# Kernel optimization log

Hardware: AMD Instinct MI355X
Metric: run time of the kernel (lower is better)

## Reference

```python
import jax, jax.numpy as jnp
import numpy as np

B, N, M, D = 4, 256, 256, 524
EPS = 1e-8


def setup_inputs() -> dict:
    key = jax.random.key(0)
    ks = jax.random.split(key, 16)

    def lin(k, fin, fout):
        kw, kb = jax.random.split(k)
        w = jax.random.normal(kw, (fin, fout), jnp.float32) * (1.0 / np.sqrt(fin))
        b = jax.random.normal(kb, (fout,), jnp.float32) * 0.01
        return w, b

    cw1, cb1 = lin(ks[3], D, 256)
    cw2, cb2 = lin(ks[4], 256, 128)
    cw3, cb3 = lin(ks[5], 128, 1)
    ow1, ob1 = lin(ks[6], D, 128)
    ow2, ob2 = lin(ks[7], 128, 1)
    return {
        "L_bat": jax.random.normal(ks[0], (B, N, M, D), jnp.float32),
        "src_centroids": jax.random.normal(ks[1], (B, N, 3), jnp.float32),
        "tgt_centroids": jax.random.normal(ks[2], (B, M, 3), jnp.float32),
        "cw1": cw1, "cb1": cb1, "cw2": cw2, "cb2": cb2, "cw3": cw3, "cb3": cb3,
        "ow1": ow1, "ob1": ob1, "ow2": ow2, "ob2": ob2,
    }


def _rot_mat_to_quat(R):
    # Shepperd's method, fully batched, scalar-last [x, y, z, w].
    tr = R[:, 0, 0] + R[:, 1, 1] + R[:, 2, 2]
    s0 = jnp.sqrt(jnp.maximum(tr + 1.0, 1e-10)) * 2
    q0 = jnp.stack([(R[:, 2, 1] - R[:, 1, 2]) / s0, (R[:, 0, 2] - R[:, 2, 0]) / s0,
                    (R[:, 1, 0] - R[:, 0, 1]) / s0, 0.25 * s0], axis=-1)
    s1 = jnp.sqrt(jnp.maximum(1.0 + R[:, 0, 0] - R[:, 1, 1] - R[:, 2, 2], 1e-10)) * 2
    q1 = jnp.stack([0.25 * s1, (R[:, 0, 1] + R[:, 1, 0]) / s1,
                    (R[:, 0, 2] + R[:, 2, 0]) / s1, (R[:, 2, 1] - R[:, 1, 2]) / s1], axis=-1)
    s2 = jnp.sqrt(jnp.maximum(1.0 + R[:, 1, 1] - R[:, 0, 0] - R[:, 2, 2], 1e-10)) * 2
    q2 = jnp.stack([(R[:, 0, 1] + R[:, 1, 0]) / s2, 0.25 * s2,
                    (R[:, 1, 2] + R[:, 2, 1]) / s2, (R[:, 0, 2] - R[:, 2, 0]) / s2], axis=-1)
    s3 = jnp.sqrt(jnp.maximum(1.0 + R[:, 2, 2] - R[:, 0, 0] - R[:, 1, 1], 1e-10)) * 2
    q3 = jnp.stack([(R[:, 0, 2] + R[:, 2, 0]) / s3, (R[:, 1, 2] + R[:, 2, 1]) / s3,
                    0.25 * s3, (R[:, 1, 0] - R[:, 0, 1]) / s3], axis=-1)
    c1 = (tr > 0)[:, None]
    c2 = ((R[:, 0, 0] > R[:, 1, 1]) & (R[:, 0, 0] > R[:, 2, 2]))[:, None]
    c3 = (R[:, 1, 1] > R[:, 2, 2])[:, None]
    q = jnp.where(c1, q0, jnp.where(c2, q1, jnp.where(c3, q2, q3)))
    return q / jnp.maximum(jnp.linalg.norm(q, axis=-1, keepdims=True), 1e-12)


def _forward(L_bat, src_centroids, tgt_centroids,
             cw1, cb1, cw2, cb2, cw3, cb3, ow1, ob1, ow2, ob2):
    # corr MLP: [B,N,M,D] -> [B,N,M]
    h = jax.nn.relu(L_bat @ cw1 + cb1)
    h = jax.nn.relu(h @ cw2 + cb2)
    corr_scores = (h @ cw3 + cb3)[..., 0]
    corr_weights = jax.nn.softmax(corr_scores, axis=2)              # softmax over M
    matched = jnp.einsum('bnmd,bnm->bnd', L_bat, corr_weights)      # [B,N,D]
    overlap = jax.nn.sigmoid(jax.nn.relu(matched @ ow1 + ob1) @ ow2 + ob2)  # [B,N,1]
    tgt_matched = jnp.einsum('bnm,bmc->bnc', corr_weights, tgt_centroids)   # [B,N,3]
    w = overlap[..., 0]
    w_norm = w / jnp.maximum(w.sum(axis=1, keepdims=True), EPS)
    src_bar = jnp.einsum('bn,bnc->bc', w_norm, src_centroids)
    tgt_bar = jnp.einsum('bn,bnc->bc', w_norm, tgt_matched)
    src_c = src_centroids - src_bar[:, None, :]
    tgt_c = tgt_matched - tgt_bar[:, None, :]
    H = jnp.einsum('bnc,bn,bnd->bcd', src_c, w_norm, tgt_c)          # [B,3,3]
    U, S, Vh = jnp.linalg.svd(H)
    R_raw = jnp.einsum('bki,bjk->bij', Vh, U)                        # Vh^T @ U^T
    det_sign = jnp.sign(jnp.linalg.det(R_raw))
    corr_fix = jnp.stack([jnp.ones_like(det_sign), jnp.ones_like(det_sign), det_sign], axis=-1)
    Vh_fix = Vh * corr_fix[:, :, None]
    R = jnp.einsum('bki,bjk->bij', Vh_fix, U)
    translation = tgt_bar - jnp.einsum('bij,bj->bi', R, src_bar)
    quaternion = _rot_mat_to_quat(R)
    return quaternion, translation, R, corr_weights, overlap


def reference(L_bat, src_centroids, tgt_centroids,
              cw1, cb1, cw2, cb2, cw3, cb3, ow1, ob1, ow2, ob2):
    return _forward(L_bat, src_centroids, tgt_centroids,
                    cw1, cb1, cw2, cb2, cw3, cb3, ow1, ob1, ow2, ob2)
```

## Files before the change

kernel.cpp:

```cpp
#include <hip/hip_runtime.h>
#include <hip/hip_bf16.h>


#define D_ 524
#define CW_OFF 64
#define OV_OFF 262208

typedef __attribute__((ext_vector_type(8))) short short8;
typedef __attribute__((ext_vector_type(4))) float floatx4;

__device__ __forceinline__ short f2bf(float v) {
  unsigned u = __builtin_bit_cast(unsigned, v);
  unsigned r = (u + 0x7FFFu + ((u >> 16) & 1u)) >> 16;
  return (short)(unsigned short)r;
}
__device__ __forceinline__ float bf2f(short s) {
  unsigned u = ((unsigned)(unsigned short)s) << 16;
  return __builtin_bit_cast(float, u);
}

__global__ void prep_kernel(const float* __restrict__ cw1, const float* __restrict__ cw2,
                            short* __restrict__ w1h, short* __restrict__ w1l,
                            short* __restrict__ w2h, short* __restrict__ w2l) {
  int t = blockIdx.x * 256 + threadIdx.x;
  if (t < 17408) {
    int lane = t & 63, ct = (t >> 6) & 15, kk = t >> 10;
    int col = ct * 16 + (lane & 15);
    int kbase = kk * 32 + ((lane >> 4) << 3);
#pragma unroll
    for (int i = 0; i < 8; ++i) {
      int k = kbase + i;
      float v = (k < D_) ? cw1[k * 256 + col] : 0.f;
      short h = f2bf(v);
      w1h[t * 8 + i] = h;
      w1l[t * 8 + i] = f2bf(v - bf2f(h));
    }
  } else if (t < 21504) {
    int u = t - 17408;
    int lane = u & 63, ct = (u >> 6) & 7, kk = u >> 9;
    int col = ct * 16 + (lane & 15);
    int kbase = kk * 32 + ((lane >> 4) << 3);
#pragma unroll
    for (int i = 0; i < 8; ++i) {
      int k = kbase + i;
      float v = cw2[k * 128 + col];
      short h = f2bf(v);
      w2h[u * 8 + i] = h;
      w2l[u * 8 + i] = f2bf(v - bf2f(h));
    }
  }
}

__global__ __launch_bounds__(256, 2) void main_kernel(
    const float* __restrict__ L, const float* __restrict__ tgt,
    const float* __restrict__ cb1, const float* __restrict__ cb2,
    const float* __restrict__ cw3, const float* __restrict__ cb3,
    const float* __restrict__ ow1, const float* __restrict__ ob1,
    const float* __restrict__ ow2, const float* __restrict__ ob2,
    const short8* __restrict__ w1h, const short8* __restrict__ w1l,
    const short8* __restrict__ w2h, const short8* __restrict__ w2l,
    float* __restrict__ out, float* __restrict__ tgtm) {
  int bn = blockIdx.x;
  int b = bn >> 8;
  int t = threadIdx.x;
  int w = t >> 6, lane = t & 63, l15 = lane & 15, q = lane >> 4;

  __shared__ __attribute__((aligned(16))) short Ah[2][64 * 72];
  __shared__ __attribute__((aligned(16))) short h1s[64 * 264];
  __shared__ float p_all[256];
  __shared__ float redw[256];
  __shared__ float ovp[256];
  __shared__ float m_s[524];
  __shared__ float o1s[128];
  __shared__ float sS;

  const float* Lbn = L + (size_t)bn * (256 * D_);
  float mac0 = 0.f, mac1 = 0.f, mac2 = 0.f;

  int srow = t >> 2, sko = (t & 3) * 16;

#pragma unroll 1
  for (int mt = 0; mt < 4; ++mt) {
    int m0 = mt * 64;
    const float* Lrow = Lbn + (size_t)(m0 + srow) * D_;

    floatx4 acc[4][4];
#pragma unroll
    for (int r = 0; r < 4; ++r)
#pragma unroll
      for (int c = 0; c < 4; ++c) acc[r][c] = (floatx4)(0.f);

    {
      floatx4 v0 = *(const floatx4*)(Lrow + sko);
      floatx4 v1 = *(const floatx4*)(Lrow + sko + 4);
      floatx4 v2 = *(const floatx4*)(Lrow + sko + 8);
      floatx4 v3 = *(const floatx4*)(Lrow + sko + 12);
      short8 sv0, sv1;
#pragma unroll
      for (int j = 0; j < 4; ++j) {
        sv0[j] = f2bf(v0[j]); sv0[4 + j] = f2bf(v1[j]);
        sv1[j] = f2bf(v2[j]); sv1[4 + j] = f2bf(v3[j]);
      }
      *(short8*)&Ah[0][srow * 72 + sko] = sv0;
      *(short8*)&Ah[0][srow * 72 + sko + 8] = sv1;
    }
    __syncthreads();

#pragma unroll 1
    for (int s = 0; s < 9; ++s) {
      int cb = s & 1;
      floatx4 nva, nvb, nvc, nvd;
      if (s < 7) {
        const float* src = Lrow + (s + 1) * 64 + sko;
        nva = *(const floatx4*)(src);
        nvb = *(const floatx4*)(src + 4);
        nvc = *(const floatx4*)(src + 8);
        nvd = *(const floatx4*)(src + 12);
      } else if (s == 7) {
#pragma unroll
        for (int j = 0; j < 4; ++j) {
          int k = 512 + sko + j;
          nva[j] = (k < D_) ? Lrow[k] : 0.f;
          nvb[j] = (k + 4 < D_) ? Lrow[k + 4] : 0.f;
          nvc[j] = (k + 8 < D_) ? Lrow[k + 8] : 0.f;
          nvd[j] = (k + 12 < D_) ? Lrow[k + 12] : 0.f;
        }
      }
      int kk0 = 2 * s;
      short8 bh0[4], bl0[4], bh1[4], bl1[4];
#pragma unroll
      for (int c = 0; c < 4; ++c) {
        int f = (kk0 * 16 + (w * 4 + c)) * 64 + lane;
        bh0[c] = w1h[f];
        bl0[c] = w1l[f];
      }
      if (s < 8) {
#pragma unroll
        for (int c = 0; c < 4; ++c) {
          int f = ((kk0 + 1) * 16 + (w * 4 + c)) * 64 + lane;
          bh1[c] = w1h[f];
          bl1[c] = w1l[f];
        }
      }
      short8 af[4];
#pragma unroll
      for (int r = 0; r < 4; ++r)
        af[r] = *(const short8*)&Ah[cb][(r * 16 + l15) * 72 + q * 8];
#pragma unroll
      for (int r = 0; r < 4; ++r)
#pragma unroll
        for (int c = 0; c < 4; ++c) {
          acc[r][c] = __builtin_amdgcn_mfma_f32_16x16x32_bf16(af[r], bh0[c], acc[r][c], 0, 0, 0);
          acc[r][c] = __builtin_amdgcn_mfma_f32_16x16x32_bf16(af[r], bl0[c], acc[r][c], 0, 0, 0);
        }
      if (s < 8) {
#pragma unroll
        for (int r = 0; r < 4; ++r)
          af[r] = *(const short8*)&Ah[cb][(r * 16 + l15) * 72 + 32 + q * 8];
#pragma unroll
        for (int r = 0; r < 4; ++r)
#pragma unroll
          for (int c = 0; c < 4; ++c) {
            acc[r][c] = __builtin_amdgcn_mfma_f32_16x16x32_bf16(af[r], bh1[c], acc[r][c], 0, 0, 0);
            acc[r][c] = __builtin_amdgcn_mfma_f32_16x16x32_bf16(af[r], bl1[c], acc[r][c], 0, 0, 0);
          }
        short8 sv0, sv1;
#pragma unroll
        for (int j = 0; j < 4; ++j) {
          sv0[j] = f2bf(nva[j]); sv0[4 + j] = f2bf(nvb[j]);
          sv1[j] = f2bf(nvc[j]); sv1[4 + j] = f2bf(nvd[j]);
        }
        *(short8*)&Ah[cb ^ 1][srow * 72 + sko] = sv0;
        *(short8*)&Ah[cb ^ 1][srow * 72 + sko + 8] = sv1;
      }
      __syncthreads();
    }

#pragma unroll
    for (int c = 0; c < 4; ++c) {
      int col = (w * 4 + c) * 16 + l15;
      float b1 = cb1[col];
#pragma unroll
      for (int r = 0; r < 4; ++r)
#pragma unroll
        for (int i = 0; i < 4; ++i) {
          int row = r * 16 + q * 4 + i;
          h1s[row * 264 + col] = f2bf(fmaxf(acc[r][c][i] + b1, 0.f));
        }
    }
    __syncthreads();

    floatx4 ac2[4][2];
#pragma unroll
    for (int r = 0; r < 4; ++r)
#pragma unroll
      for (int c = 0; c < 2; ++c) ac2[r][c] = (floatx4)(0.f);
#pragma unroll 2
    for (int kk = 0; kk < 8; ++kk) {
      short8 a2[4];
#pragma unroll
      for (int r = 0; r < 4; ++r)
        a2[r] = *(const short8*)&h1s[(r * 16 + l15) * 264 + kk * 32 + q * 8];
      short8 b2h_[2], b2l_[2];
#pragma unroll
      for (int c = 0; c < 2; ++c) {
        int f = (kk * 8 + (w * 2 + c)) * 64 + lane;
        b2h_[c] = w2h[f];
        b2l_[c] = w2l[f];
      }
#pragma unroll
      for (int r = 0; r < 4; ++r)
#pragma unroll
        for (int c = 0; c < 2; ++c) {
          ac2[r][c] = __builtin_amdgcn_mfma_f32_16x16x32_bf16(a2[r], b2h_[c], ac2[r][c], 0, 0, 0);
          ac2[r][c] = __builtin_amdgcn_mfma_f32_16x16x32_bf16(a2[r], b2l_[c], ac2[r][c], 0, 0, 0);
        }
    }

    float pr[4][4];
#pragma unroll
    for (int r = 0; r < 4; ++r)
#pragma unroll
      for (int i = 0; i < 4; ++i) pr[r][i] = 0.f;
#pragma unroll
    for (int c = 0; c < 2; ++c) {
      int col = (w * 2 + c) * 16 + l15;
      float b2 = cb2[col], w3 = cw3[col];
#pragma unroll
      for (int r = 0; r < 4; ++r)
#pragma unroll
        for (int i = 0; i < 4; ++i)
          pr[r][i] += fmaxf(ac2[r][c][i] + b2, 0.f) * w3;
    }
#pragma unroll
    for (int m = 1; m <= 8; m <<= 1)
#pragma unroll
      for (int r = 0; r < 4; ++r)
#pragma unroll
        for (int i = 0; i < 4; ++i) pr[r][i] += __shfl_xor(pr[r][i], m, 64);
    if (l15 == 0) {
#pragma unroll
      for (int r = 0; r < 4; ++r)
#pragma unroll
        for (int i = 0; i < 4; ++i) redw[w * 64 + r * 16 + q * 4 + i] = pr[r][i];
    }
    __syncthreads();
    if (t < 64) {
      float s = redw[t] + redw[64 + t] + redw[128 + t] + redw[192 + t] + cb3[0];
      p_all[m0 + t] = expf(s);
    }
    __syncthreads();

#pragma unroll 8
    for (int m = 0; m < 64; ++m) {
      float pm = p_all[m0 + m];
      const float* Lr = Lbn + (size_t)(m0 + m) * D_;
      mac0 += pm * Lr[t];
      mac1 += pm * Lr[t + 256];
      if (t < 12) mac2 += pm * Lr[t + 512];
    }
  }

  if (t < 64) {
    float v = p_all[t] + p_all[t + 64] + p_all[t + 128] + p_all[t + 192];
#pragma unroll
    for (int m = 1; m <= 32; m <<= 1) v += __shfl_xor(v, m, 64);
    if (t == 0) sS = 1.f / v;
  }
  __syncthreads();
  float invS = sS;
  out[CW_OFF + bn * 256 + t] = p_all[t] * invS;
  m_s[t] = mac0 * invS;
  m_s[t + 256] = mac1 * invS;
  if (t < 12) m_s[t + 512] = mac2 * invS;
  __syncthreads();

  {
    int o = t & 127, half = t >> 7;
    float a = 0.f;
#pragma unroll 4
    for (int dd = 0; dd < 262; ++dd) {
      int d = half * 262 + dd;
      a += m_s[d] * ow1[d * 128 + o];
    }
    ovp[t] = a;
  }
  if (t < 96) {
    int c = t % 3, g = t / 3;
    float s = 0.f;
#pragma unroll
    for (int m = 0; m < 8; ++m) s += p_all[g * 8 + m] * tgt[((b * 256) + g * 8 + m) * 3 + c];
    redw[t] = s;
  }
  __syncthreads();
  if (t < 128) o1s[t] = fmaxf(ovp[t] + ovp[t + 128] + ob1[t], 0.f) * ow2[t];
  __syncthreads();
  if (t < 64) {
    float v = o1s[t] + o1s[t + 64];
#pragma unroll
    for (int m = 1; m <= 32; m <<= 1) v += __shfl_xor(v, m, 64);
    if (t == 0) out[OV_OFF + bn] = 1.f / (1.f + expf(-(v + ob2[0])));
  }
  if (t < 3) {
    float s = 0.f;
    for (int g = 0; g < 32; ++g) s += redw[g * 3 + t];
    tgtm[bn * 3 + t] = s * invS;
  }
}

__global__ __launch_bounds__(256) void finalize_kernel(const float* __restrict__ src,
                                                       const float* __restrict__ tgtm,
                                                       float* __restrict__ out) {
  int b = blockIdx.x, t = threadIdx.x;
  __shared__ float red[256];

  auto bsum = [&](float v) -> float {
    red[t] = v;
    __syncthreads();
    for (int s = 128; s > 0; s >>= 1) {
      if (t < s) red[t] += red[t + s];
      __syncthreads();
    }
    float r = red[0];
    __syncthreads();
    return r;
  };

  float wv = out[OV_OFF + b * 256 + t];
  float Sw = bsum(wv);
  float wn = wv / fmaxf(Sw, 1e-8f);
  float sc[3], tm[3];
#pragma unroll
  for (int c = 0; c < 3; ++c) {
    sc[c] = src[(b * 256 + t) * 3 + c];
    tm[c] = tgtm[(b * 256 + t) * 3 + c];
  }
  float sb[3], tb[3];
#pragma unroll
  for (int c = 0; c < 3; ++c) sb[c] = bsum(wn * sc[c]);
#pragma unroll
  for (int c = 0; c < 3; ++c) tb[c] = bsum(wn * tm[c]);
  float Hv[9];
#pragma unroll
  for (int c = 0; c < 3; ++c)
#pragma unroll
    for (int d = 0; d < 3; ++d)
      Hv[c * 3 + d] = bsum((sc[c] - sb[c]) * wn * (tm[d] - tb[d]));

  if (t == 0) {
    double H[3][3];
    for (int i = 0; i < 3; ++i)
      for (int j = 0; j < 3; ++j) H[i][j] = (double)Hv[i * 3 + j];
    double A[3][3], V[3][3] = {{1, 0, 0}, {0, 1, 0}, {0, 0, 1}};
    for (int i = 0; i < 3; ++i)
      for (int j = 0; j < 3; ++j) {
        double s = 0;
        for (int k = 0; k < 3; ++k) s += H[k][i] * H[k][j];
        A[i][j] = s;
      }
    const int PQ[3][2] = {{0, 1}, {0, 2}, {1, 2}};
    for (int sweep = 0; sweep < 30; ++sweep)
      for (int r = 0; r < 3; ++r) {
        int p = PQ[r][0], qq = PQ[r][1];
        double apq = A[p][qq];
        if (fabs(apq) < 1e-300) continue;
        double tau = (A[qq][qq] - A[p][p]) / (2.0 * apq);
        double tt = (tau >= 0 ? 1.0 : -1.0) / (fabs(tau) + sqrt(1.0 + tau * tau));
        double cc = 1.0 / sqrt(1.0 + tt * tt), ss = tt * cc;
        for (int k = 0; k < 3; ++k) {
          double akp = A[k][p], akq = A[k][qq];
          A[k][p] = cc * akp - ss * akq;
          A[k][qq] = ss * akp + cc * akq;
        }
        for (int k = 0; k < 3; ++k) {
          double apk = A[p][k], aqk = A[qq][k];
          A[p][k] = cc * apk - ss * aqk;
          A[qq][k] = ss * apk + cc * aqk;
        }
        for (int k = 0; k < 3; ++k) {
          double vkp = V[k][p], vkq = V[k][qq];
          V[k][p] = cc * vkp - ss * vkq;
          V[k][qq] = ss * vkp + cc * vkq;
        }
      }
    int idx[3] = {0, 1, 2};
    for (int i = 0; i < 2; ++i)
      for (int j = i + 1; j < 3; ++j)
        if (A[idx[j]][idx[j]] > A[idx[i]][idx[i]]) { int tmp = idx[i]; idx[i] = idx[j]; idx[j] = tmp; }
    double v0[3], v1[3], v2[3];
    for (int k = 0; k < 3; ++k) {
      v0[k] = V[k][idx[0]];
      v1[k] = V[k][idx[1]];
      v2[k] = V[k][idx[2]];
    }
    double u0[3], u1[3], u2[3];
    for (int j = 0; j < 3; ++j) {
      u0[j] = H[j][0] * v0[0] + H[j][1] * v0[1] + H[j][2] * v0[2];
      u1[j] = H[j][0] * v1[0] + H[j][1] * v1[1] + H[j][2] * v1[2];
    }
    double n0 = sqrt(u0[0] * u0[0] + u0[1] * u0[1] + u0[2] * u0[2]);
    n0 = (n0 > 1e-300) ? n0 : 1e-300;
    for (int j = 0; j < 3; ++j) u0[j] /= n0;
    double d01 = u0[0] * u1[0] + u0[1] * u1[1] + u0[2] * u1[2];
    for (int j = 0; j < 3; ++j) u1[j] -= d01 * u0[j];
    double n1 = sqrt(u1[0] * u1[0] + u1[1] * u1[1] + u1[2] * u1[2]);
    n1 = (n1 > 1e-300) ? n1 : 1e-300;
    for (int j = 0; j < 3; ++j) u1[j] /= n1;
    u2[0] = u0[1] * u1[2] - u0[2] * u1[1];
    u2[1] = u0[2] * u1[0] - u0[0] * u1[2];
    u2[2] = u0[0] * u1[1] - u0[1] * u1[0];
    double Rr[3][3];
    for (int i = 0; i < 3; ++i)
      for (int j = 0; j < 3; ++j)
        Rr[i][j] = v0[i] * u0[j] + v1[i] * u1[j] + v2[i] * u2[j];
    double det = Rr[0][0] * (Rr[1][1] * Rr[2][2] - Rr[1][2] * Rr[2][1]) -
                 Rr[0][1] * (Rr[1][0] * Rr[2][2] - Rr[1][2] * Rr[2][0]) +
                 Rr[0][2] * (Rr[1][0] * Rr[2][1] - Rr[1][1] * Rr[2][0]);
    double sg = (det >= 0) ? 1.0 : -1.0;
    double R[3][3];
    for (int i = 0; i < 3; ++i)
      for (int j = 0; j < 3; ++j)
        R[i][j] = v0[i] * u0[j] + v1[i] * u1[j] + sg * v2[i] * u2[j];
    double trv[3];
    for (int i = 0; i < 3; ++i)
      trv[i] = (double)tb[i] - (R[i][0] * sb[0] + R[i][1] * sb[1] + R[i][2] * sb[2]);
    double qv[4];
    double tr = R[0][0] + R[1][1] + R[2][2];
    if (tr > 0) {
      double S = sqrt(fmax(tr + 1.0, 1e-10)) * 2.0;
      qv[0] = (R[2][1] - R[1][2]) / S;
      qv[1] = (R[0][2] - R[2][0]) / S;
      qv[2] = (R[1][0] - R[0][1]) / S;
      qv[3] = 0.25 * S;
    } else if (R[0][0] > R[1][1] && R[0][0] > R[2][2]) {
      double S = sqrt(fmax(1.0 + R[0][0] - R[1][1] - R[2][2], 1e-10)) * 2.0;
      qv[0] = 0.25 * S;
      qv[1] = (R[0][1] + R[1][0]) / S;
      qv[2] = (R[0][2] + R[2][0]) / S;
      qv[3] = (R[2][1] - R[1][2]) / S;
    } else if (R[1][1] > R[2][2]) {
      double S = sqrt(fmax(1.0 + R[1][1] - R[0][0] - R[2][2], 1e-10)) * 2.0;
      qv[0] = (R[0][1] + R[1][0]) / S;
      qv[1] = 0.25 * S;
      qv[2] = (R[1][2] + R[2][1]) / S;
      qv[3] = (R[0][2] - R[2][0]) / S;
    } else {
      double S = sqrt(fmax(1.0 + R[2][2] - R[0][0] - R[1][1], 1e-10)) * 2.0;
      qv[0] = (R[0][2] + R[2][0]) / S;
      qv[1] = (R[1][2] + R[2][1]) / S;
      qv[2] = 0.25 * S;
      qv[3] = (R[1][0] - R[0][1]) / S;
    }
    double qn = sqrt(qv[0] * qv[0] + qv[1] * qv[1] + qv[2] * qv[2] + qv[3] * qv[3]);
    qn = fmax(qn, 1e-12);
    for (int k = 0; k < 4; ++k) out[b * 4 + k] = (float)(qv[k] / qn);
    for (int i = 0; i < 3; ++i) out[16 + b * 3 + i] = (float)trv[i];
    for (int i = 0; i < 3; ++i)
      for (int j = 0; j < 3; ++j) out[28 + b * 9 + i * 3 + j] = (float)R[i][j];
  }
}

extern "C" void kernel_launch(void* const* d_in, const int* in_sizes, int n_in,
                              void* d_out, int out_size, void* d_ws, size_t ws_size,
                              hipStream_t stream) {
  const float* L = (const float*)d_in[0];
  const float* src = (const float*)d_in[1];
  const float* tgt = (const float*)d_in[2];
  const float* cw1 = (const float*)d_in[3];
  const float* cb1 = (const float*)d_in[4];
  const float* cw2 = (const float*)d_in[5];
  const float* cb2 = (const float*)d_in[6];
  const float* cw3 = (const float*)d_in[7];
  const float* cb3 = (const float*)d_in[8];
  const float* ow1 = (const float*)d_in[9];
  const float* ob1 = (const float*)d_in[10];
  const float* ow2 = (const float*)d_in[11];
  const float* ob2 = (const float*)d_in[12];
  float* out = (float*)d_out;

  char* ws = (char*)d_ws;
  short* w1h = (short*)(ws);
  short* w1l = (short*)(ws + 278528);
  short* w2h = (short*)(ws + 557056);
  short* w2l = (short*)(ws + 622592);
  float* tgtm = (float*)(ws + 688128);

  hipLaunchKernelGGL(prep_kernel, dim3(84), dim3(256), 0, stream, cw1, cw2, w1h, w1l, w2h, w2l);
  hipLaunchKernelGGL(main_kernel, dim3(1024), dim3(256), 0, stream,
                     L, tgt, cb1, cb2, cw3, cb3, ow1, ob1, ow2, ob2,
                     (const short8*)w1h, (const short8*)w1l,
                     (const short8*)w2h, (const short8*)w2l, out, tgtm);
  hipLaunchKernelGGL(finalize_kernel, dim3(4), dim3(256), 0, stream, src, tgtm, out);
}
```

Before: 1.111 ms.

## Load L fragments directly from global into MFMA registers, drop LDS staging

Removes the double-buffered LDS staging of the bf16-converted L tile. Each wave now loads its A fragments straight from global memory into registers and converts them there, so the per-step __syncthreads are gone. LDS use drops, and launch bounds are raised to 4 blocks per CU for more occupancy. In exchange, the four waves each re-read the same L rows from global/L2 (about 4x redundant traffic), loads are strided per lane and less coalesced, and there is no explicit prefetch.

New measurement: 1.281 ms. +15.3%, slower.

```diff
diff --git a/kernel.cpp b/kernel.cpp
--- a/kernel.cpp
+++ b/kernel.cpp
@@ -51,7 +51,7 @@
   }
 }
 
-__global__ __launch_bounds__(256, 2) void main_kernel(
+__global__ __launch_bounds__(256, 4) void main_kernel(
     const float* __restrict__ L, const float* __restrict__ tgt,
     const float* __restrict__ cb1, const float* __restrict__ cb2,
     const float* __restrict__ cw3, const float* __restrict__ cb3,
@@ -65,7 +65,6 @@
   int t = threadIdx.x;
   int w = t >> 6, lane = t & 63, l15 = lane & 15, q = lane >> 4;
 
-  __shared__ __attribute__((aligned(16))) short Ah[2][64 * 72];
   __shared__ __attribute__((aligned(16))) short h1s[64 * 264];
   __shared__ float p_all[256];
   __shared__ float redw[256];
@@ -77,12 +76,14 @@
   const float* Lbn = L + (size_t)bn * (256 * D_);
   float mac0 = 0.f, mac1 = 0.f, mac2 = 0.f;
 
-  int srow = t >> 2, sko = (t & 3) * 16;
-
 #pragma unroll 1
   for (int mt = 0; mt < 4; ++mt) {
     int m0 = mt * 64;
-    const float* Lrow = Lbn + (size_t)(m0 + srow) * D_;
+
+    const float* Ar0 = Lbn + (size_t)(m0 + l15) * D_;
+    const float* Ar1 = Ar0 + 16 * D_;
+    const float* Ar2 = Ar0 + 32 * D_;
+    const float* Ar3 = Ar0 + 48 * D_;
 
     floatx4 acc[4][4];
 #pragma unroll
@@ -90,90 +91,63 @@
 #pragma unroll
       for (int c = 0; c < 4; ++c) acc[r][c] = (floatx4)(0.f);
 
+#pragma unroll 1
+    for (int kk = 0; kk < 16; ++kk) {
+      int kc = kk * 32 + q * 8;
+      short8 bh[4], bl[4];
+#pragma unroll
+      for (int c = 0; c < 4; ++c) {
+        int f = (kk * 16 + (w * 4 + c)) * 64 + lane;
+        bh[c] = w1h[f];
+        bl[c] = w1l[f];
+      }
+      short8 af[4];
+#pragma unroll
+      for (int r = 0; r < 4; ++r) {
+        const float* Ar = (r == 0) ? Ar0 : (r == 1) ? Ar1 : (r == 2) ? Ar2 : Ar3;
+        floatx4 a0 = *(const floatx4*)(Ar + kc);
+        floatx4 a1 = *(const floatx4*)(Ar + kc + 4);
+        short8 v;
+#pragma unroll
+        for (int j = 0; j < 4; ++j) { v[j] = f2bf(a0[j]); v[4 + j] = f2bf(a1[j]); }
+        af[r] = v;
+      }
+#pragma unroll
+      for (int r = 0; r < 4; ++r)
+#pragma unroll
+        for (int c = 0; c < 4; ++c) {
+          acc[r][c] = __builtin_amdgcn_mfma_f32_16x16x32_bf16(af[r], bh[c], acc[r][c], 0, 0, 0);
+          acc[r][c] = __builtin_amdgcn_mfma_f32_16x16x32_bf16(af[r], bl[c], acc[r][c], 0, 0, 0);
+        }
+    }
     {
-      floatx4 v0 = *(const floatx4*)(Lrow + sko);
-      floatx4 v1 = *(const floatx4*)(Lrow + sko + 4);
-      floatx4 v2 = *(const floatx4*)(Lrow + sko + 8);
-      floatx4 v3 = *(const floatx4*)(Lrow + sko + 12);
-      short8 sv0, sv1;
-#pragma unroll
-      for (int j = 0; j < 4; ++j) {
-        sv0[j] = f2bf(v0[j]); sv0[4 + j] = f2bf(v1[j]);
-        sv1[j] = f2bf(v2[j]); sv1[4 + j] = f2bf(v3[j]);
-      }
-      *(short8*)&Ah[0][srow * 72 + sko] = sv0;
-      *(short8*)&Ah[0][srow * 72 + sko + 8] = sv1;
-    }
-    __syncthreads();
-
-#pragma unroll 1
-    for (int s = 0; s < 9; ++s) {
-      int cb = s & 1;
-      floatx4 nva, nvb, nvc, nvd;
-      if (s < 7) {
-        const float* src = Lrow + (s + 1) * 64 + sko;
-        nva = *(const floatx4*)(src);
-        nvb = *(const floatx4*)(src + 4);
-        nvc = *(const floatx4*)(src + 8);
-        nvd = *(const floatx4*)(src + 12);
-      } else if (s == 7) {
-#pragma unroll
-        for (int j = 0; j < 4; ++j) {
-          int k = 512 + sko + j;
-          nva[j] = (k < D_) ? Lrow[k] : 0.f;
-          nvb[j] = (k + 4 < D_) ? Lrow[k + 4] : 0.f;
-          nvc[j] = (k + 8 < D_) ? Lrow[k + 8] : 0.f;
-          nvd[j] = (k + 12 < D_) ? Lrow[k + 12] : 0.f;
-        }
-      }
-      int kk0 = 2 * s;
-      short8 bh0[4], bl0[4], bh1[4], bl1[4];
+      short8 bh[4], bl[4];
 #pragma unroll
       for (int c = 0; c < 4; ++c) {
-        int f = (kk0 * 16 + (w * 4 + c)) * 64 + lane;
-        bh0[c] = w1h[f];
-        bl0[c] = w1l[f];
-      }
-      if (s < 8) {
+        int f = (256 + (w * 4 + c)) * 64 + lane;
+        bh[c] = w1h[f];
+        bl[c] = w1l[f];
+      }
+      short8 af[4];
+#pragma unroll
+      for (int r = 0; r < 4; ++r) {
+        const float* Ar = (r == 0) ? Ar0 : (r == 1) ? Ar1 : (r == 2) ? Ar2 : Ar3;
+        short8 v;
+#pragma unroll
+        for (int i = 0; i < 8; ++i) {
+          int k = 512 + q * 8 + i;
+          float x = (k < D_) ? Ar[k] : 0.f;
+          v[i] = f2bf(x);
+        }
+        af[r] = v;
+      }
+#pragma unroll
+      for (int r = 0; r < 4; ++r)
 #pragma unroll
         for (int c = 0; c < 4; ++c) {
-          int f = ((kk0 + 1) * 16 + (w * 4 + c)) * 64 + lane;
-          bh1[c] = w1h[f];
-          bl1[c] = w1l[f];
-        }
-      }
-      short8 af[4];
-#pragma unroll
-      for (int r = 0; r < 4; ++r)
-        af[r] = *(const short8*)&Ah[cb][(r * 16 + l15) * 72 + q * 8];
-#pragma unroll
-      for (int r = 0; r < 4; ++r)
-#pragma unroll
-        for (int c = 0; c < 4; ++c) {
-          acc[r][c] = __builtin_amdgcn_mfma_f32_16x16x32_bf16(af[r], bh0[c], acc[r][c], 0, 0, 0);
-          acc[r][c] = __builtin_amdgcn_mfma_f32_16x16x32_bf16(af[r], bl0[c], acc[r][c], 0, 0, 0);
-        }
-      if (s < 8) {
-#pragma unroll
-        for (int r = 0; r < 4; ++r)
-          af[r] = *(const short8*)&Ah[cb][(r * 16 + l15) * 72 + 32 + q * 8];
-#pragma unroll
-        for (int r = 0; r < 4; ++r)
-#pragma unroll
-          for (int c = 0; c < 4; ++c) {
-            acc[r][c] = __builtin_amdgcn_mfma_f32_16x16x32_bf16(af[r], bh1[c], acc[r][c], 0, 0, 0);
-            acc[r][c] = __builtin_amdgcn_mfma_f32_16x16x32_bf16(af[r], bl1[c], acc[r][c], 0, 0, 0);
-          }
-        short8 sv0, sv1;
-#pragma unroll
-        for (int j = 0; j < 4; ++j) {
-          sv0[j] = f2bf(nva[j]); sv0[4 + j] = f2bf(nvb[j]);
-          sv1[j] = f2bf(nvc[j]); sv1[4 + j] = f2bf(nvd[j]);
-        }
-        *(short8*)&Ah[cb ^ 1][srow * 72 + sko] = sv0;
-        *(short8*)&Ah[cb ^ 1][srow * 72 + sko + 8] = sv1;
-      }
-      __syncthreads();
+          acc[r][c] = __builtin_amdgcn_mfma_f32_16x16x32_bf16(af[r], bh[c], acc[r][c], 0, 0, 0);
+          acc[r][c] = __builtin_amdgcn_mfma_f32_16x16x32_bf16(af[r], bl[c], acc[r][c], 0, 0, 0);
+        }
     }
 
 #pragma unroll
```
